# Performance work log

Measured on AMD Instinct MI355X. Metric: run time of the kernel, lower is better.

The kernel has to match this reference:

```python
import jax, jax.numpy as jnp
import numpy as np

N = 20000
E = 400000
LATENT = 128
HIDDEN = 512
OUT = 64
HEADS = 4
NEG_SLOPE = 0.2


def setup_inputs() -> dict:
    key = jax.random.key(0)
    ks = jax.random.split(key, 12)
    z = jax.random.normal(ks[0], (N, LATENT), dtype=jnp.float32)
    edge_index = jax.random.randint(ks[1], (2, E), 0, N, dtype=jnp.int64)
    h1 = HIDDEN // 2
    # dense1, dense2 (torch Linear: y = x @ W.T + b; store W already transposed)
    W1 = jax.random.normal(ks[2], (LATENT, h1), dtype=jnp.float32) / np.sqrt(LATENT)
    b1 = jnp.zeros((h1,), dtype=jnp.float32)
    W2 = jax.random.normal(ks[3], (h1, HIDDEN), dtype=jnp.float32) / np.sqrt(h1)
    b2 = jnp.zeros((HIDDEN,), dtype=jnp.float32)
    # GATConv params
    Wg = jax.random.normal(ks[4], (HIDDEN, HEADS * OUT), dtype=jnp.float32) / np.sqrt(HIDDEN)
    att_src = jax.random.normal(ks[5], (HEADS, OUT), dtype=jnp.float32) * 0.1
    att_dst = jax.random.normal(ks[6], (HEADS, OUT), dtype=jnp.float32) * 0.1
    bias_g = jnp.zeros((OUT,), dtype=jnp.float32)
    return {"z": z, "W1": W1, "b1": b1, "W2": W2, "b2": b2,
            "Wg": Wg, "att_src": att_src, "att_dst": att_dst, "bias_g": bias_g,
            "edge_index": edge_index}


def _gat(x, Wg, att_src, att_dst, bias_g, src, dst):
    # project: [N, H, D]
    h = (x @ Wg).reshape(N, HEADS, OUT)
    a_src = jnp.einsum('nhd,hd->nh', h, att_src)  # [N, H]
    a_dst = jnp.einsum('nhd,hd->nh', h, att_dst)
    e = a_src[src] + a_dst[dst]                   # [E+N, H]
    e = jax.nn.leaky_relu(e, NEG_SLOPE)
    # segment softmax over destination nodes
    m = jax.ops.segment_max(e, dst, num_segments=N)
    e = jnp.exp(e - m[dst])
    denom = jax.ops.segment_sum(e, dst, num_segments=N)
    w = e / (denom[dst] + 1e-16)                  # [E+N, H]
    msg = h[src] * w[:, :, None]                  # [E+N, H, D]
    out = jax.ops.segment_sum(msg, dst, num_segments=N)  # [N, H, D]
    return out.mean(axis=1) + bias_g              # concat=False -> mean heads


def reference(z, W1, b1, W2, b2, Wg, att_src, att_dst, bias_g, edge_index):
    x = jax.nn.relu(z @ W1 + b1)
    x = jax.nn.relu(x @ W2 + b2)
    # PyG GATConv default add_self_loops=True
    loop = jnp.arange(N, dtype=edge_index.dtype)
    src = jnp.concatenate([edge_index[0], loop])
    dst = jnp.concatenate([edge_index[1], loop])
    return _gat(x, Wg, att_src, att_dst, bias_g, src, dst)
```

## Files before the change

### kernel.cpp

```cpp
#include <hip/hip_runtime.h>
#include <hip/hip_bf16.h>

#define N_NODES 20000
#define MPAD    20096
#define E_EDGES 400000
#define LATENT 128
#define H1 256
#define HIDDEN 512
#define OUT_D 64
#define HEADS 4
#define NEG_SLOPE 0.2f
#define MAX_IN 80

typedef __attribute__((ext_vector_type(8))) __bf16 bf16x8;
typedef __attribute__((ext_vector_type(4))) float f32x4;
typedef __attribute__((ext_vector_type(4))) unsigned short u16x4;

__device__ __forceinline__ unsigned short f2bf(float f) {
    union { float f; unsigned int u; } v; v.f = f;
    unsigned int r = v.u + 0x7fffu + ((v.u >> 16) & 1u);
    return (unsigned short)(r >> 16);
}
__device__ __forceinline__ float bf2f(unsigned short u) {
    union { unsigned int u; float f; } v; v.u = ((unsigned int)u) << 16;
    return v.f;
}

#define SEG1 (LATENT * H1)
#define SEG2 (H1 * HIDDEN)
#define SEG3 (HIDDEN * HEADS * OUT_D)
#define WTOT (SEG1 + SEG2 + SEG3)
__global__ __launch_bounds__(256)
void prep_kernel(const float* __restrict__ W1, const float* __restrict__ W2,
                 const float* __restrict__ Wg,
                 unsigned short* __restrict__ W1t, unsigned short* __restrict__ W2t,
                 unsigned short* __restrict__ Wgt, int* __restrict__ cur) {
    int t = blockIdx.x * blockDim.x + threadIdx.x;
    if (t < SEG1) { int k = t >> 8, n = t & 255; W1t[n * LATENT + k] = f2bf(W1[t]); return; }
    t -= SEG1;
    if (t < SEG2) { int k = t >> 9, n = t & 511; W2t[n * H1 + k] = f2bf(W2[t]); return; }
    t -= SEG2;
    if (t < SEG3) { int k = t >> 8, n = t & 255; Wgt[n * HIDDEN + k] = f2bf(Wg[t]); return; }
    t -= SEG3;
    if (t < N_NODES) cur[t] = 0;
}

#define TM 32
#define ZPITCH 136
#define XPITCH 264
#define X2PITCH 520
#define MLP_BLOCKS (MPAD / TM)
#define SCAT_BLOCKS ((E_EDGES + 255) / 256)
__global__ __launch_bounds__(256, 4)
void mlp_scatter_kernel(const float* __restrict__ z,
                        const unsigned short* __restrict__ W1t,
                        const unsigned short* __restrict__ W2t,
                        const unsigned short* __restrict__ Wgt,
                        const float* __restrict__ b1, const float* __restrict__ b2,
                        const float* __restrict__ att_src, const float* __restrict__ att_dst,
                        const int* __restrict__ ei, int* __restrict__ cur,
                        int* __restrict__ adj,
                        unsigned short* __restrict__ hb,
                        float* __restrict__ a_src, float* __restrict__ a_dst) {
    __shared__ unsigned short x2s[TM * X2PITCH];
    __shared__ unsigned short x1s[TM * XPITCH];

    if (blockIdx.x >= MLP_BLOCKS) {
        int t = (blockIdx.x - MLP_BLOCKS) * 256 + threadIdx.x;
        if (t < E_EDGES) {
            int s = ei[t], d = ei[E_EDGES + t];
            int idx = atomicAdd(&cur[d], 1);
            idx = min(idx, MAX_IN - 1);
            adj[d * MAX_IN + idx] = s;
        }
        return;
    }

    unsigned short* zbf = x2s;
    const int tid = threadIdx.x;
    const int wave = tid >> 6, lane = tid & 63;
    const int m0 = blockIdx.x * TM;
    const int fr = lane & 15, q = lane >> 4;

#define LDW1(kt, t)      (*(const bf16x8*)(W1t + (size_t)(nb1 + (t) * 16 + fr) * LATENT + (kt) * 32 + q * 8))
#define LDW2H(nh, kt, t) (*(const bf16x8*)(W2t + (size_t)(nb2 + (nh) * 64 + (t) * 16 + fr) * H1 + (kt) * 32 + q * 8))
#define LDW3(kt, t)      (*(const bf16x8*)(Wgt + (size_t)(nb3 + (t) * 16 + fr) * HIDDEN + (kt) * 32 + q * 8))

    const int nb1 = wave * 64;
    const int nb2 = wave * 128;
    const int head = wave;
    const int nb3 = wave * 64;

    bf16x8 w1a[4], w1b[4];
#pragma unroll
    for (int t = 0; t < 4; t++) w1a[t] = LDW1(0, t);

    {
        const int r = tid >> 3, c0 = (tid & 7) * 16;
        const int zrow = min(m0 + r, N_NODES - 1);
        const float* zp = z + (size_t)zrow * LATENT + c0;
#pragma unroll
        for (int i = 0; i < 4; i++) {
            f32x4 v = *(const f32x4*)(zp + i * 4);
            u16x4 p = { f2bf(v[0]), f2bf(v[1]), f2bf(v[2]), f2bf(v[3]) };
            *(u16x4*)(zbf + r * ZPITCH + c0 + i * 4) = p;
        }
    }
    __syncthreads();

    f32x4 acc1[2][4] = {};
#pragma unroll
    for (int kt = 0; kt < 4; kt++) {
        bf16x8* wc = (kt & 1) ? w1b : w1a;
        bf16x8* wn = (kt & 1) ? w1a : w1b;
        if (kt < 3) {
#pragma unroll
            for (int t = 0; t < 4; t++) wn[t] = LDW1(kt + 1, t);
        }
        bf16x8 af[2];
#pragma unroll
        for (int t = 0; t < 2; t++)
            af[t] = *(const bf16x8*)(zbf + (t * 16 + fr) * ZPITCH + kt * 32 + q * 8);
#pragma unroll
        for (int mt = 0; mt < 2; mt++)
#pragma unroll
            for (int nt = 0; nt < 4; nt++)
                acc1[mt][nt] = __builtin_amdgcn_mfma_f32_16x16x32_bf16(
                    wc[nt], af[mt], acc1[mt][nt], 0, 0, 0);
    }

    bf16x8 w2a[4], w2b[4];
#pragma unroll
    for (int t = 0; t < 4; t++) w2a[t] = LDW2H(0, 0, t);

#pragma unroll
    for (int nt = 0; nt < 4; nt++) {
        const int n = nb1 + nt * 16 + q * 4;
        const f32x4 bv = *(const f32x4*)(b1 + n);
#pragma unroll
        for (int mt = 0; mt < 2; mt++) {
            u16x4 p;
#pragma unroll
            for (int r = 0; r < 4; r++) p[r] = f2bf(fmaxf(acc1[mt][nt][r] + bv[r], 0.f));
            *(u16x4*)(x1s + (mt * 16 + fr) * XPITCH + n) = p;
        }
    }
    __syncthreads();

#pragma unroll
    for (int nh = 0; nh < 2; nh++) {
        if (nh == 1) {
#pragma unroll
            for (int t = 0; t < 4; t++) w2a[t] = LDW2H(1, 0, t);
        }
        f32x4 acc2[2][4] = {};
#pragma unroll
        for (int kt = 0; kt < 8; kt++) {
            bf16x8* wc = (kt & 1) ? w2b : w2a;
            bf16x8* wn = (kt & 1) ? w2a : w2b;
            if (kt < 7) {
#pragma unroll
                for (int t = 0; t < 4; t++) wn[t] = LDW2H(nh, kt + 1, t);
            }
            bf16x8 af[2];
#pragma unroll
            for (int t = 0; t < 2; t++)
                af[t] = *(const bf16x8*)(x1s + (t * 16 + fr) * XPITCH + kt * 32 + q * 8);
#pragma unroll
            for (int mt = 0; mt < 2; mt++)
#pragma unroll
                for (int nt = 0; nt < 4; nt++)
                    acc2[mt][nt] = __builtin_amdgcn_mfma_f32_16x16x32_bf16(
                        wc[nt], af[mt], acc2[mt][nt], 0, 0, 0);
        }
#pragma unroll
        for (int nt = 0; nt < 4; nt++) {
            const int n = nb2 + nh * 64 + nt * 16 + q * 4;
            const f32x4 bv = *(const f32x4*)(b2 + n);
#pragma unroll
            for (int mt = 0; mt < 2; mt++) {
                u16x4 p;
#pragma unroll
                for (int r = 0; r < 4; r++) p[r] = f2bf(fmaxf(acc2[mt][nt][r] + bv[r], 0.f));
                *(u16x4*)(x2s + (mt * 16 + fr) * X2PITCH + n) = p;
            }
        }
    }

    bf16x8 w3a[4], w3b[4];
#pragma unroll
    for (int t = 0; t < 4; t++) w3a[t] = LDW3(0, t);
    __syncthreads();

    f32x4 acc3[2][4] = {};
#pragma unroll
    for (int kt = 0; kt < 16; kt++) {
        bf16x8* wc = (kt & 1) ? w3b : w3a;
        bf16x8* wn = (kt & 1) ? w3a : w3b;
        if (kt < 15) {
#pragma unroll
            for (int t = 0; t < 4; t++) wn[t] = LDW3(kt + 1, t);
        }
        bf16x8 af[2];
#pragma unroll
        for (int t = 0; t < 2; t++)
            af[t] = *(const bf16x8*)(x2s + (t * 16 + fr) * X2PITCH + kt * 32 + q * 8);
#pragma unroll
        for (int mt = 0; mt < 2; mt++)
#pragma unroll
            for (int nt = 0; nt < 4; nt++)
                acc3[mt][nt] = __builtin_amdgcn_mfma_f32_16x16x32_bf16(
                    wc[nt], af[mt], acc3[mt][nt], 0, 0, 0);
    }

    {
        f32x4 asv[4], adv[4];
#pragma unroll
        for (int nt = 0; nt < 4; nt++) {
            asv[nt] = *(const f32x4*)(att_src + head * OUT_D + nt * 16 + q * 4);
            adv[nt] = *(const f32x4*)(att_dst + head * OUT_D + nt * 16 + q * 4);
        }
#pragma unroll
        for (int mt = 0; mt < 2; mt++) {
            const int row = m0 + mt * 16 + fr;
            float vs = 0.f, vd = 0.f;
#pragma unroll
            for (int nt = 0; nt < 4; nt++) {
                u16x4 p;
#pragma unroll
                for (int r = 0; r < 4; r++) {
                    float x = acc3[mt][nt][r];
                    p[r] = f2bf(x);
                    vs += x * asv[nt][r];
                    vd += x * adv[nt][r];
                }
                *(u16x4*)(hb + (size_t)row * (HEADS * OUT_D) + head * OUT_D + nt * 16 + q * 4) = p;
            }
            vs += __shfl_xor(vs, 16, 64); vs += __shfl_xor(vs, 32, 64);
            vd += __shfl_xor(vd, 16, 64); vd += __shfl_xor(vd, 32, 64);
            if (q == 0 && row < N_NODES) {
                a_src[row * HEADS + head] = vs;
                a_dst[row * HEADS + head] = vd;
            }
        }
    }
#undef LDW1
#undef LDW2H
#undef LDW3
}

__global__ __launch_bounds__(256) void fused_gat(const int* __restrict__ adj,
                                                 const int* __restrict__ cur,
                                                 const float* __restrict__ a_src,
                                                 const float* __restrict__ a_dst,
                                                 const unsigned short* __restrict__ hb,
                                                 const float* __restrict__ bias_g,
                                                 float* __restrict__ out) {
    const int wave = threadIdx.x >> 6, lane = threadIdx.x & 63;
    const int d = blockIdx.x * 4 + wave;
    const int h = lane >> 4, j = lane & 15;
    const int cnt = min(cur[d], MAX_IN);
    const int* arow = adj + d * MAX_IN;

    __shared__ float lw[4][HEADS][32];
    __shared__ int   si[4][32];

    const float ad = a_dst[d * HEADS + h];

    float vself = a_src[d * HEADS + h] + ad;
    vself = (vself > 0.f) ? vself : NEG_SLOPE * vself;
    const float wself = __expf(fminf(vself, 60.f));

    float sm = 0.f;
    for (int e = j; e < cnt; e += 16) {
        int s = arow[e];
        float v = a_src[s * HEADS + h] + ad;
        v = (v > 0.f) ? v : NEG_SLOPE * v;
        float ex = __expf(fminf(v, 60.f));
        if (e < 32) {
            lw[wave][h][e] = ex;
            if (h == 0) si[wave][e] = s;
        }
        sm += ex;
    }
#pragma unroll
    for (int off = 1; off < 16; off <<= 1) sm += __shfl_xor(sm, off, 64);
    const float inv = 1.f / (sm + wself + 1e-16f);

    const unsigned short* hp = hb + h * OUT_D + j * 4;
    u16x4 gself = *(const u16x4*)(hp + (size_t)d * (HEADS * OUT_D));
    float a0 = wself * bf2f(gself[0]), a1 = wself * bf2f(gself[1]);
    float a2 = wself * bf2f(gself[2]), a3 = wself * bf2f(gself[3]);

    const int lim = cnt < 32 ? cnt : 32;
    int e = 0;
    for (; e + 7 < lim; e += 8) {
        int   sx[8]; float wx[8]; u16x4 gx[8];
#pragma unroll
        for (int u = 0; u < 8; u++) { sx[u] = si[wave][e + u]; wx[u] = lw[wave][h][e + u]; }
#pragma unroll
        for (int u = 0; u < 8; u++) gx[u] = *(const u16x4*)(hp + (size_t)sx[u] * (HEADS * OUT_D));
#pragma unroll
        for (int u = 0; u < 8; u++) {
            a0 += wx[u] * bf2f(gx[u][0]); a1 += wx[u] * bf2f(gx[u][1]);
            a2 += wx[u] * bf2f(gx[u][2]); a3 += wx[u] * bf2f(gx[u][3]);
        }
    }
    for (; e + 3 < lim; e += 4) {
        int   sx[4]; float wx[4]; u16x4 gx[4];
#pragma unroll
        for (int u = 0; u < 4; u++) { sx[u] = si[wave][e + u]; wx[u] = lw[wave][h][e + u]; }
#pragma unroll
        for (int u = 0; u < 4; u++) gx[u] = *(const u16x4*)(hp + (size_t)sx[u] * (HEADS * OUT_D));
#pragma unroll
        for (int u = 0; u < 4; u++) {
            a0 += wx[u] * bf2f(gx[u][0]); a1 += wx[u] * bf2f(gx[u][1]);
            a2 += wx[u] * bf2f(gx[u][2]); a3 += wx[u] * bf2f(gx[u][3]);
        }
    }
    for (; e < lim; e++) {
        int s = si[wave][e];
        float w = lw[wave][h][e];
        u16x4 g = *(const u16x4*)(hp + (size_t)s * (HEADS * OUT_D));
        a0 += w * bf2f(g[0]); a1 += w * bf2f(g[1]);
        a2 += w * bf2f(g[2]); a3 += w * bf2f(g[3]);
    }
    for (int e2 = 32; e2 < cnt; e2++) {
        int s = arow[e2];
        float v = a_src[s * HEADS + h] + ad;
        v = (v > 0.f) ? v : NEG_SLOPE * v;
        float w = __expf(fminf(v, 60.f));
        u16x4 g = *(const u16x4*)(hp + (size_t)s * (HEADS * OUT_D));
        a0 += w * bf2f(g[0]); a1 += w * bf2f(g[1]);
        a2 += w * bf2f(g[2]); a3 += w * bf2f(g[3]);
    }
    a0 *= inv; a1 *= inv; a2 *= inv; a3 *= inv;

    a0 += __shfl_xor(a0, 16, 64); a0 += __shfl_xor(a0, 32, 64);
    a1 += __shfl_xor(a1, 16, 64); a1 += __shfl_xor(a1, 32, 64);
    a2 += __shfl_xor(a2, 16, 64); a2 += __shfl_xor(a2, 32, 64);
    a3 += __shfl_xor(a3, 16, 64); a3 += __shfl_xor(a3, 32, 64);
    if (lane < 16) {
        f32x4 bg = *(const f32x4*)(bias_g + lane * 4);
        f32x4 r = { 0.25f * a0 + bg[0], 0.25f * a1 + bg[1],
                    0.25f * a2 + bg[2], 0.25f * a3 + bg[3] };
        *(f32x4*)(out + (size_t)d * OUT_D + lane * 4) = r;
    }
}

extern "C" void kernel_launch(void* const* d_in, const int* in_sizes, int n_in,
                              void* d_out, int out_size, void* d_ws, size_t ws_size,
                              hipStream_t stream) {
    const float* z       = (const float*)d_in[0];
    const float* W1      = (const float*)d_in[1];
    const float* b1      = (const float*)d_in[2];
    const float* W2      = (const float*)d_in[3];
    const float* b2      = (const float*)d_in[4];
    const float* Wg      = (const float*)d_in[5];
    const float* att_src = (const float*)d_in[6];
    const float* att_dst = (const float*)d_in[7];
    const float* bias_g  = (const float*)d_in[8];
    const int*   ei      = (const int*)d_in[9];
    float* out = (float*)d_out;

    char* ws = (char*)d_ws;
    size_t off = 0;
    auto carve = [&](size_t bytes) { void* p = ws + off; off += (bytes + 255) & ~(size_t)255; return p; };

    unsigned short* W1t = (unsigned short*)carve((size_t)H1 * LATENT * 2);
    unsigned short* W2t = (unsigned short*)carve((size_t)HIDDEN * H1 * 2);
    unsigned short* Wgt = (unsigned short*)carve((size_t)(HEADS * OUT_D) * HIDDEN * 2);
    unsigned short* hb  = (unsigned short*)carve((size_t)MPAD * HEADS * OUT_D * 2);
    float* a_src = (float*)carve((size_t)N_NODES * HEADS * 4);
    float* a_dst = (float*)carve((size_t)N_NODES * HEADS * 4);
    int*   cur   = (int*)carve((size_t)N_NODES * 4);
    int*   adj   = (int*)carve((size_t)MAX_IN * N_NODES * 4);

    prep_kernel<<<(WTOT + N_NODES + 255) / 256, 256, 0, stream>>>(
        W1, W2, Wg, W1t, W2t, Wgt, cur);

    mlp_scatter_kernel<<<MLP_BLOCKS + SCAT_BLOCKS, 256, 0, stream>>>(
        z, W1t, W2t, Wgt, b1, b2, att_src, att_dst, ei, cur, adj, hb, a_src, a_dst);

    fused_gat<<<N_NODES / 4, 256, 0, stream>>>(
        adj, cur, a_src, a_dst, hb, bias_g, out);
}
```

Baseline: 163.8 us.

## Process two destination nodes per wave with single-pass softmax aggregation

```diff
diff --git a/kernel.cpp b/kernel.cpp
--- a/kernel.cpp
+++ b/kernel.cpp
@@ -15,6 +15,7 @@
 typedef __attribute__((ext_vector_type(8))) __bf16 bf16x8;
 typedef __attribute__((ext_vector_type(4))) float f32x4;
 typedef __attribute__((ext_vector_type(4))) unsigned short u16x4;
+typedef __attribute__((ext_vector_type(8))) unsigned short u16x8;
 
 __device__ __forceinline__ unsigned short f2bf(float f) {
     union { float f; unsigned int u; } v; v.f = f;
@@ -249,102 +250,93 @@
 #undef LDW3
 }
 
-__global__ __launch_bounds__(256) void fused_gat(const int* __restrict__ adj,
-                                                 const int* __restrict__ cur,
-                                                 const float* __restrict__ a_src,
-                                                 const float* __restrict__ a_dst,
-                                                 const unsigned short* __restrict__ hb,
-                                                 const float* __restrict__ bias_g,
-                                                 float* __restrict__ out) {
+__global__ __launch_bounds__(256)
+void fused_gat(const int* __restrict__ adj, const int* __restrict__ cur,
+               const float* __restrict__ a_src, const float* __restrict__ a_dst,
+               const unsigned short* __restrict__ hb,
+               const float* __restrict__ bias_g, float* __restrict__ out) {
     const int wave = threadIdx.x >> 6, lane = threadIdx.x & 63;
-    const int d = blockIdx.x * 4 + wave;
-    const int h = lane >> 4, j = lane & 15;
+    const int grp = lane >> 5, sl = lane & 31;
+    const int d = blockIdx.x * 8 + wave * 2 + grp;
+    const int h = sl >> 3, j = sl & 7;
     const int cnt = min(cur[d], MAX_IN);
     const int* arow = adj + d * MAX_IN;
 
-    __shared__ float lw[4][HEADS][32];
-    __shared__ int   si[4][32];
-
     const float ad = a_dst[d * HEADS + h];
+    const unsigned short* hp = hb + h * OUT_D + j * 8;
 
     float vself = a_src[d * HEADS + h] + ad;
     vself = (vself > 0.f) ? vself : NEG_SLOPE * vself;
-    const float wself = __expf(fminf(vself, 60.f));
-
-    float sm = 0.f;
-    for (int e = j; e < cnt; e += 16) {
+    float sm = __expf(fminf(vself, 60.f));
+    u16x8 gs = *(const u16x8*)(hp + (size_t)d * (HEADS * OUT_D));
+    float acc[8];
+#pragma unroll
+    for (int r = 0; r < 8; r++) acc[r] = sm * bf2f(gs[r]);
+
+    int e = 0;
+    for (; e + 7 < cnt; e += 8) {
+        int sx[8]; float fx[8]; u16x8 gx[8];
+#pragma unroll
+        for (int u = 0; u < 8; u++) sx[u] = arow[e + u];
+#pragma unroll
+        for (int u = 0; u < 8; u++) fx[u] = a_src[sx[u] * HEADS + h];
+#pragma unroll
+        for (int u = 0; u < 8; u++) gx[u] = *(const u16x8*)(hp + (size_t)sx[u] * (HEADS * OUT_D));
+#pragma unroll
+        for (int u = 0; u < 8; u++) {
+            float v = fx[u] + ad;
+            v = (v > 0.f) ? v : NEG_SLOPE * v;
+            float w = __expf(fminf(v, 60.f));
+            sm += w;
+#pragma unroll
+            for (int r = 0; r < 8; r++) acc[r] += w * bf2f(gx[u][r]);
+        }
+    }
+    for (; e + 3 < cnt; e += 4) {
+        int sx[4]; float fx[4]; u16x8 gx[4];
+#pragma unroll
+        for (int u = 0; u < 4; u++) sx[u] = arow[e + u];
+#pragma unroll
+        for (int u = 0; u < 4; u++) fx[u] = a_src[sx[u] * HEADS + h];
+#pragma unroll
+        for (int u = 0; u < 4; u++) gx[u] = *(const u16x8*)(hp + (size_t)sx[u] * (HEADS * OUT_D));
+#pragma unroll
+        for (int u = 0; u < 4; u++) {
+            float v = fx[u] + ad;
+            v = (v > 0.f) ? v : NEG_SLOPE * v;
+            float w = __expf(fminf(v, 60.f));
+            sm += w;
+#pragma unroll
+            for (int r = 0; r < 8; r++) acc[r] += w * bf2f(gx[u][r]);
+        }
+    }
+    for (; e < cnt; e++) {
         int s = arow[e];
         float v = a_src[s * HEADS + h] + ad;
         v = (v > 0.f) ? v : NEG_SLOPE * v;
-        float ex = __expf(fminf(v, 60.f));
-        if (e < 32) {
-            lw[wave][h][e] = ex;
-            if (h == 0) si[wave][e] = s;
-        }
-        sm += ex;
-    }
-#pragma unroll
-    for (int off = 1; off < 16; off <<= 1) sm += __shfl_xor(sm, off, 64);
-    const float inv = 1.f / (sm + wself + 1e-16f);
-
-    const unsigned short* hp = hb + h * OUT_D + j * 4;
-    u16x4 gself = *(const u16x4*)(hp + (size_t)d * (HEADS * OUT_D));
-    float a0 = wself * bf2f(gself[0]), a1 = wself * bf2f(gself[1]);
-    float a2 = wself * bf2f(gself[2]), a3 = wself * bf2f(gself[3]);
-
-    const int lim = cnt < 32 ? cnt : 32;
-    int e = 0;
-    for (; e + 7 < lim; e += 8) {
-        int   sx[8]; float wx[8]; u16x4 gx[8];
-#pragma unroll
-        for (int u = 0; u < 8; u++) { sx[u] = si[wave][e + u]; wx[u] = lw[wave][h][e + u]; }
-#pragma unroll
-        for (int u = 0; u < 8; u++) gx[u] = *(const u16x4*)(hp + (size_t)sx[u] * (HEADS * OUT_D));
-#pragma unroll
-        for (int u = 0; u < 8; u++) {
-            a0 += wx[u] * bf2f(gx[u][0]); a1 += wx[u] * bf2f(gx[u][1]);
-            a2 += wx[u] * bf2f(gx[u][2]); a3 += wx[u] * bf2f(gx[u][3]);
-        }
-    }
-    for (; e + 3 < lim; e += 4) {
-        int   sx[4]; float wx[4]; u16x4 gx[4];
-#pragma unroll
-        for (int u = 0; u < 4; u++) { sx[u] = si[wave][e + u]; wx[u] = lw[wave][h][e + u]; }
-#pragma unroll
-        for (int u = 0; u < 4; u++) gx[u] = *(const u16x4*)(hp + (size_t)sx[u] * (HEADS * OUT_D));
-#pragma unroll
-        for (int u = 0; u < 4; u++) {
-            a0 += wx[u] * bf2f(gx[u][0]); a1 += wx[u] * bf2f(gx[u][1]);
-            a2 += wx[u] * bf2f(gx[u][2]); a3 += wx[u] * bf2f(gx[u][3]);
-        }
-    }
-    for (; e < lim; e++) {
-        int s = si[wave][e];
-        float w = lw[wave][h][e];
-        u16x4 g = *(const u16x4*)(hp + (size_t)s * (HEADS * OUT_D));
-        a0 += w * bf2f(g[0]); a1 += w * bf2f(g[1]);
-        a2 += w * bf2f(g[2]); a3 += w * bf2f(g[3]);
-    }
-    for (int e2 = 32; e2 < cnt; e2++) {
-        int s = arow[e2];
-        float v = a_src[s * HEADS + h] + ad;
-        v = (v > 0.f) ? v : NEG_SLOPE * v;
         float w = __expf(fminf(v, 60.f));
-        u16x4 g = *(const u16x4*)(hp + (size_t)s * (HEADS * OUT_D));
-        a0 += w * bf2f(g[0]); a1 += w * bf2f(g[1]);
-        a2 += w * bf2f(g[2]); a3 += w * bf2f(g[3]);
-    }
-    a0 *= inv; a1 *= inv; a2 *= inv; a3 *= inv;
-
-    a0 += __shfl_xor(a0, 16, 64); a0 += __shfl_xor(a0, 32, 64);
-    a1 += __shfl_xor(a1, 16, 64); a1 += __shfl_xor(a1, 32, 64);
-    a2 += __shfl_xor(a2, 16, 64); a2 += __shfl_xor(a2, 32, 64);
-    a3 += __shfl_xor(a3, 16, 64); a3 += __shfl_xor(a3, 32, 64);
-    if (lane < 16) {
-        f32x4 bg = *(const f32x4*)(bias_g + lane * 4);
-        f32x4 r = { 0.25f * a0 + bg[0], 0.25f * a1 + bg[1],
-                    0.25f * a2 + bg[2], 0.25f * a3 + bg[3] };
-        *(f32x4*)(out + (size_t)d * OUT_D + lane * 4) = r;
+        u16x8 g = *(const u16x8*)(hp + (size_t)s * (HEADS * OUT_D));
+        sm += w;
+#pragma unroll
+        for (int r = 0; r < 8; r++) acc[r] += w * bf2f(g[r]);
+    }
+
+    const float inv = 1.f / (sm + 1e-16f);
+#pragma unroll
+    for (int r = 0; r < 8; r++) {
+        acc[r] *= inv;
+        acc[r] += __shfl_xor(acc[r], 8, 64);
+        acc[r] += __shfl_xor(acc[r], 16, 64);
+    }
+    if (h == 0) {
+        const f32x4 bg0 = *(const f32x4*)(bias_g + j * 8);
+        const f32x4 bg1 = *(const f32x4*)(bias_g + j * 8 + 4);
+        f32x4 o0 = { 0.25f * acc[0] + bg0[0], 0.25f * acc[1] + bg0[1],
+                     0.25f * acc[2] + bg0[2], 0.25f * acc[3] + bg0[3] };
+        f32x4 o1 = { 0.25f * acc[4] + bg1[0], 0.25f * acc[5] + bg1[1],
+                     0.25f * acc[6] + bg1[2], 0.25f * acc[7] + bg1[3] };
+        *(f32x4*)(out + (size_t)d * OUT_D + j * 8) = o0;
+        *(f32x4*)(out + (size_t)d * OUT_D + j * 8 + 4) = o1;
     }
 }
 
@@ -382,6 +374,6 @@
     mlp_scatter_kernel<<<MLP_BLOCKS + SCAT_BLOCKS, 256, 0, stream>>>(
         z, W1t, W2t, Wgt, b1, b2, att_src, att_dst, ei, cur, adj, hb, a_src, a_dst);
 
-    fused_gat<<<N_NODES / 4, 256, 0, stream>>>(
+    fused_gat<<<N_NODES / 8, 256, 0, stream>>>(
         adj, cur, a_src, a_dst, hb, bias_g, out);
 }
```

Result: slower. 167.1 us (+2.1%).
